# Kernel optimization log

Measured on AMD Instinct MI355X. Metric: run time of the kernel, lower is better.

The kernel has to match this reference:

```python
import jax, jax.numpy as jnp
import numpy as np

B, IN, H, OUT, RANK = 2048, 256, 128, 128, 8
EPS = 1e-5

def setup_inputs() -> dict:
    key = jax.random.key(0)
    ks = jax.random.split(key, 9)
    inv = lambda n: 1.0 / np.sqrt(n)
    return {
        "X": jax.random.normal(ks[0], (B, IN), jnp.float32),
        "W1": jax.random.uniform(ks[1], (IN, H), jnp.float32, -inv(IN), inv(IN)),
        "b1": jnp.zeros((H,), jnp.float32),
        "W2": jax.random.uniform(ks[2], (IN, OUT), jnp.float32, -inv(IN), inv(IN)),
        "b2": jnp.zeros((OUT,), jnp.float32),
        "W3": jax.random.uniform(ks[3], (H, OUT), jnp.float32, -inv(H), inv(H)),
        "b3": jnp.zeros((OUT,), jnp.float32),
        "P": jax.random.normal(ks[4], (RANK, H, H, H), jnp.float32),  # (rank, p, q, k)
        "gz": jnp.ones((H,), jnp.float32),
        "bz": jnp.zeros((H,), jnp.float32),
        "gy": jnp.ones((H,), jnp.float32),
        "by": jnp.zeros((H,), jnp.float32),
    }

def _bn(x, g, b):
    # training-mode BatchNorm1d: batch stats, biased variance
    m = x.mean(axis=0)
    v = x.var(axis=0)
    return (x - m) * jax.lax.rsqrt(v + EPS) * g + b

def reference(X, W1, b1, W2, b2, W3, b3, P, gz, bz, gy, by):
    Z = jax.nn.relu(X @ W1 + b1)               # (B, H); dropout = identity (eval)

    def step(carry, Pi):
        Zi, Y = carry
        # batch_quadratic: out[b,k] = sum_{p,q} Zi[b,p] * Pi[p,q,k] * Z[b,q]
        Zi = jnp.einsum('bp,pqk,bq->bk', Zi, Pi, Z)
        Zi = _bn(Zi, gz, bz)
        return (Zi, Y + Zi / RANK), None

    Y0 = jnp.zeros((X.shape[0], H), X.dtype)
    (_, Y), _ = jax.lax.scan(step, (Z, Y0), P)
    Y = _bn(Y, gy, by)
    out = jax.nn.relu(jax.nn.relu(Y @ W3 + b3) + jax.nn.relu(X @ W2 + b2))
    return out
```

## Files before the change

### kernel.cpp

```cpp
#include <hip/hip_runtime.h>

typedef __bf16 bf16x8 __attribute__((ext_vector_type(8)));
typedef float  floatx4 __attribute__((ext_vector_type(4)));

constexpr int B_    = 2048;
constexpr int NIN   = 256;
constexpr int H_    = 128;
constexpr int RANK_ = 8;
constexpr float EPS_ = 1e-5f;
constexpr int MT    = 32;
constexpr int SZS   = 36;

__global__ __launch_bounds__(256)
void k_head(const float* __restrict__ X,
            const float* __restrict__ W1, const float* __restrict__ b1,
            const float* __restrict__ W2, const float* __restrict__ b2,
            const float* __restrict__ P,
            float* __restrict__ Z, float* __restrict__ R2, __bf16* __restrict__ Zbf,
            __bf16* __restrict__ Pperm, float* __restrict__ stats ) {
    __shared__ float smem[512];
    const int bx = blockIdx.x, t = threadIdx.x;

    if (bx < RANK_ + 1) stats[bx * 256 + t] = 0.f;

    if (bx < 512) {
        const int col = t & 127, half = t >> 7;
        for (int it = 0; it < 2; ++it) {
            const int row0 = bx * 4 + it * 2;
            smem[t]       = X[(size_t)row0       * NIN + t];
            smem[256 + t] = X[(size_t)(row0 + 1) * NIN + t];
            __syncthreads();
            float s1 = 0.f, s2 = 0.f;
            const float* sx = smem + half * 256;
#pragma unroll 8
            for (int i = 0; i < NIN; ++i) {
                s1 = fmaf(sx[i], W1[i * H_ + col], s1);
                s2 = fmaf(sx[i], W2[i * H_ + col], s2);
            }
            const int b = row0 + half;
            const float z = fmaxf(s1 + b1[col], 0.f);
            const float r = fmaxf(s2 + b2[col], 0.f);
            Z[(size_t)b * H_ + col]   = z;
            Zbf[(size_t)b * H_ + col] = (__bf16)z;
            R2[(size_t)b * H_ + col]  = r;
            __syncthreads();
        }
    }
    {
        const int s = t >> 6, Lp = t & 63, quad = Lp >> 4, lo = Lp & 15;
        const int pr = bx >> 7, p = bx & 127;
        const float* Pp = P     + ((size_t)pr * H_ + p) * (H_ * H_);
        __bf16*      dp = Pperm + ((size_t)pr * H_ + p) * (H_ * H_);
#pragma unroll
        for (int c = 0; c < 8; ++c) {
            __bf16 v[8];
#pragma unroll
            for (int jj = 0; jj < 8; ++jj)
                v[jj] = (__bf16)Pp[(s * 32 + quad * 8 + jj) * H_ + c * 16 + lo];
            *(bf16x8*)(dp + (((size_t)(s * 8 + c)) * 64 + Lp) * 8) = *(const bf16x8*)v;
        }
    }
}

__global__ __launch_bounds__(256, 2)
void k_rank(const __bf16* __restrict__ Pr, const __bf16* __restrict__ Zbf,
            const float* __restrict__ prevT, const float* __restrict__ prevStats,
            const float* __restrict__ gz, const float* __restrict__ bz,
            float* __restrict__ T, float* __restrict__ stats, const int first) {
    __shared__ float smem[4864];
    const int m = blockIdx.x, kg = blockIdx.y, b0 = m * MT;
    const int t = threadIdx.x;
    const int w = t >> 6, L = t & 63, quad = L >> 4, lo = L & 15;
    const int sp = t & 127, rg = t >> 7;

    float* sAl = smem + 4608; float* sBe = smem + 4736;
    if (t < 128) {
        if (first) { sAl[t] = 1.f; sBe[t] = 0.f; }
        else {
            const float s1 = prevStats[t], s2 = prevStats[128 + t];
            const float mm = s1 * (1.f / B_);
            const float var = s2 * (1.f / B_) - mm * mm;
            const float a = rsqrtf(var + EPS_) * gz[t];
            sAl[t] = a; sBe[t] = bz[t] - mm * a;
        }
    }
    bf16x8 A[2][4];
#pragma unroll
    for (int mt = 0; mt < 2; ++mt)
#pragma unroll
        for (int ks = 0; ks < 4; ++ks)
            A[mt][ks] = *(const bf16x8*)(Zbf + (size_t)(b0 + mt * 16 + lo) * H_ + ks * 32 + quad * 8);
    __syncthreads();
    {
        const float a = sAl[sp], be = sBe[sp];
#pragma unroll
        for (int i = 0; i < 16; ++i) {
            const int row = rg + 2 * i;
            smem[sp * SZS + row] = fmaf(prevT[(size_t)(b0 + row) * H_ + sp], a, be);
        }
    }
    __syncthreads();

    floatx4 acc[2];
    acc[0] = (floatx4){0.f, 0.f, 0.f, 0.f};
    acc[1] = (floatx4){0.f, 0.f, 0.f, 0.f};
    const bf16x8* Pb = (const bf16x8*)Pr;
    for (int pp = 0; pp < 32; ++pp) {
        const int p = pp * 4 + w;
        bf16x8 Bf[4];
#pragma unroll
        for (int s = 0; s < 4; ++s)
            Bf[s] = Pb[((size_t)(p * 4 + s) * 8 + kg) * 64 + L];
        floatx4 S[2];
        S[0] = (floatx4){0.f, 0.f, 0.f, 0.f};
        S[1] = (floatx4){0.f, 0.f, 0.f, 0.f};
#pragma unroll
        for (int ks = 0; ks < 4; ++ks)
#pragma unroll
            for (int mt = 0; mt < 2; ++mt)
                S[mt] = __builtin_amdgcn_mfma_f32_16x16x32_bf16(A[mt][ks], Bf[ks], S[mt], 0, 0, 0);
#pragma unroll
        for (int mt = 0; mt < 2; ++mt) {
            const floatx4 zi = *(const floatx4*)&smem[p * SZS + mt * 16 + quad * 4];
            acc[mt] += zi * S[mt];
        }
    }
    __syncthreads();
#pragma unroll
    for (int mt = 0; mt < 2; ++mt)
#pragma unroll
        for (int i = 0; i < 4; ++i)
            smem[w * 512 + (mt * 4 + i) * 64 + L] = acc[mt][i];
    if (t < 32) smem[2048 + t] = 0.f;
    __syncthreads();

    float cs = 0.f, cs2 = 0.f;
#pragma unroll
    for (int k2 = 0; k2 < 2; ++k2) {
        const int e = t + 256 * k2;
        const float v = smem[e] + smem[512 + e] + smem[1024 + e] + smem[1536 + e];
        const int j = e >> 6, L2 = e & 63;
        const int row = b0 + (j >> 2) * 16 + (L2 >> 4) * 4 + (j & 3);
        const int col = kg * 16 + (L2 & 15);
        T[(size_t)row * H_ + col] = v;
        cs += v; cs2 += v * v;
    }
    cs  += __shfl_xor(cs, 16);  cs  += __shfl_xor(cs, 32);
    cs2 += __shfl_xor(cs2, 16); cs2 += __shfl_xor(cs2, 32);
    if (L < 16) { atomicAdd(&smem[2048 + L], cs); atomicAdd(&smem[2064 + L], cs2); }
    __syncthreads();
    if (t < 16)      atomicAdd(&stats[kg * 16 + t],            smem[2048 + t]);
    else if (t < 32) atomicAdd(&stats[128 + kg * 16 + t - 16], smem[2048 + t]);
}

__global__ __launch_bounds__(256)
void k_y(const float* __restrict__ T, const float* __restrict__ sums,
         const float* __restrict__ gz, const float* __restrict__ bz,
         float* __restrict__ Y, float* __restrict__ ysums) {
    __shared__ float al[1024], be[1024], red[256];
    const int bx = blockIdx.x, t = threadIdx.x;
    for (int e = t; e < 1024; e += 256) {
        const int rr = e >> 7, k = e & 127;
        const float s1 = sums[rr * 256 + k], s2 = sums[rr * 256 + 128 + k];
        const float mm = s1 * (1.f / B_);
        const float var = s2 * (1.f / B_) - mm * mm;
        const float a = rsqrtf(var + EPS_) * gz[k];
        al[e] = a; be[e] = bz[k] - mm * a;
    }
    red[t] = 0.f;
    __syncthreads();
    const int col = t & 127, half = t >> 7;
    float ps = 0.f, ps2 = 0.f;
    for (int i = 0; i < 16; ++i) {
        const int b = bx * 32 + half + 2 * i;
        float y = 0.f;
#pragma unroll
        for (int rr = 0; rr < 8; ++rr)
            y += fmaf(T[(size_t)rr * B_ * H_ + (size_t)b * H_ + col],
                      al[rr * 128 + col], be[rr * 128 + col]);
        y *= (1.f / RANK_);
        Y[(size_t)b * H_ + col] = y;
        ps += y; ps2 += y * y;
    }
    atomicAdd(&red[col], half == 0 ? ps : 0.f);
    atomicAdd(&red[128 + col], half == 0 ? ps2 : 0.f);
    __syncthreads();
    atomicAdd(&red[col],       half == 1 ? ps : 0.f);
    atomicAdd(&red[128 + col], half == 1 ? ps2 : 0.f);
    __syncthreads();
    if (t < 128) {
        atomicAdd(&ysums[t],       red[t]);
        atomicAdd(&ysums[128 + t], red[128 + t]);
    }
}

__global__ void k_out(const float* __restrict__ Y, const float* __restrict__ ystats,
                      const float* __restrict__ gy, const float* __restrict__ by,
                      const float* __restrict__ W3, const float* __restrict__ b3,
                      const float* __restrict__ R2, float* __restrict__ out) {
    __shared__ float sy[H_];
    const int b = blockIdx.x, t = threadIdx.x;
    const float m  = ystats[t] * (1.f / B_);
    const float v  = ystats[128 + t] * (1.f / B_) - m * m;
    const float rs = rsqrtf(v + EPS_);
    sy[t] = (Y[(size_t)b * H_ + t] - m) * rs * gy[t] + by[t];
    __syncthreads();
    float s = 0.f;
#pragma unroll 8
    for (int h = 0; h < H_; ++h)
        s = fmaf(sy[h], W3[h * H_ + t], s);
    const float r = fmaxf(s + b3[t], 0.f) + R2[(size_t)b * H_ + t];
    out[(size_t)b * H_ + t] = fmaxf(r, 0.f);
}

extern "C" void kernel_launch(void* const* d_in, const int* in_sizes, int n_in,
                              void* d_out, int out_size, void* d_ws, size_t ws_size,
                              hipStream_t stream) {
    const float* X  = (const float*)d_in[0];
    const float* W1 = (const float*)d_in[1];
    const float* b1 = (const float*)d_in[2];
    const float* W2 = (const float*)d_in[3];
    const float* b2 = (const float*)d_in[4];
    const float* W3 = (const float*)d_in[5];
    const float* b3 = (const float*)d_in[6];
    const float* P  = (const float*)d_in[7];
    const float* gz = (const float*)d_in[8];
    const float* bz = (const float*)d_in[9];
    const float* gy = (const float*)d_in[10];
    const float* by = (const float*)d_in[11];
    float* out = (float*)d_out;

    const size_t rankElems = (size_t)H_ * H_ * H_;

    char* wsb = (char*)d_ws;
    float* Z      = (float*)wsb;   wsb += (size_t)B_ * H_ * 4;
    float* R2     = (float*)wsb;   wsb += (size_t)B_ * H_ * 4;
    float* Y      = (float*)wsb;   wsb += (size_t)B_ * H_ * 4;
    float* stats  = (float*)wsb;   wsb += (size_t)(RANK_ + 1) * 256 * 4;
    float* T      = (float*)wsb;   wsb += (size_t)RANK_ * B_ * H_ * 4;
    __bf16* Zbf   = (__bf16*)wsb;  wsb += (size_t)B_ * H_ * 2;
    __bf16* Pperm = (__bf16*)wsb;

    float* ysums = stats + RANK_ * 256;

    k_head<<<1024, 256, 0, stream>>>(X, W1, b1, W2, b2, P, Z, R2, Zbf, Pperm, stats);

    for (int r = 0; r < RANK_; ++r) {
        const float* prevT = (r == 0) ? Z : (T + (size_t)(r - 1) * B_ * H_);
        const float* prevS = (r == 0) ? stats : (stats + (r - 1) * 256);
        k_rank<<<dim3(64, 8), 256, 0, stream>>>(Pperm + (size_t)r * rankElems, Zbf,
                                                prevT, prevS, gz, bz,
                                                T + (size_t)r * B_ * H_, stats + r * 256,
                                                r == 0 ? 1 : 0);
    }

    k_y<<<64, 256, 0, stream>>>(T, stats, gz, bz, Y, ysums);
    k_out<<<B_, H_, 0, stream>>>(Y, ysums, gy, by, W3, b3, R2, out);
}
```

Baseline: 334.5 us.

## Retile rank kernel to 1024-thread blocks, coalesce P permute, batch output rows

The rank kernel now uses 1024-thread blocks covering 64 batch rows, with 16 waves split across row tiles and p slices. The grid is reordered so kg varies fastest, and the next P fragments are prefetched into registers to overlap loads with MFMA. The head kernel's P-to-bf16 permutation now reads P with coalesced float4 loads and transposes through shared memory. The head GEMM is spread over all 1024 blocks, and the output kernel handles 8 rows per block to reuse W3 loads. The larger blocks and prefetch registers may lower occupancy, and the launch bound asks for 4 blocks of 1024 threads per CU.

```diff
diff --git a/kernel.cpp b/kernel.cpp
--- a/kernel.cpp
+++ b/kernel.cpp
@@ -8,8 +8,6 @@
 constexpr int H_    = 128;
 constexpr int RANK_ = 8;
 constexpr float EPS_ = 1e-5f;
-constexpr int MT    = 32;
-constexpr int SZS   = 36;
 
 __global__ __launch_bounds__(256)
 void k_head(const float* __restrict__ X,
@@ -18,62 +16,75 @@
             const float* __restrict__ P,
             float* __restrict__ Z, float* __restrict__ R2, __bf16* __restrict__ Zbf,
             __bf16* __restrict__ Pperm, float* __restrict__ stats ) {
-    __shared__ float smem[512];
+    __shared__ __bf16 sT[128 * 40];
+    float* sx = (float*)sT;
     const int bx = blockIdx.x, t = threadIdx.x;
 
     if (bx < RANK_ + 1) stats[bx * 256 + t] = 0.f;
 
-    if (bx < 512) {
+    {
+        const int row0 = bx * 2;
+        sx[t]       = X[(size_t)row0       * NIN + t];
+        sx[256 + t] = X[(size_t)(row0 + 1) * NIN + t];
+        __syncthreads();
         const int col = t & 127, half = t >> 7;
-        for (int it = 0; it < 2; ++it) {
-            const int row0 = bx * 4 + it * 2;
-            smem[t]       = X[(size_t)row0       * NIN + t];
-            smem[256 + t] = X[(size_t)(row0 + 1) * NIN + t];
+        float s1 = 0.f, s2 = 0.f;
+        const float* sxh = sx + half * 256;
+#pragma unroll 8
+        for (int i = 0; i < NIN; ++i) {
+            s1 = fmaf(sxh[i], W1[i * H_ + col], s1);
+            s2 = fmaf(sxh[i], W2[i * H_ + col], s2);
+        }
+        const int b = row0 + half;
+        const float z = fmaxf(s1 + b1[col], 0.f);
+        const float r = fmaxf(s2 + b2[col], 0.f);
+        Z[(size_t)b * H_ + col]   = z;
+        Zbf[(size_t)b * H_ + col] = (__bf16)z;
+        R2[(size_t)b * H_ + col]  = r;
+        __syncthreads();
+    }
+    {
+        const int pr = bx >> 7, p = bx & 127;
+        const float4* Pp4 = (const float4*)(P + ((size_t)pr * H_ + p) * (H_ * H_));
+        __bf16* dp = Pperm + ((size_t)pr * H_ + p) * (H_ * H_);
+        const int L = t & 63, quad = L >> 4, lo = L & 15, c0 = t >> 6;
+#pragma unroll
+        for (int s = 0; s < 4; ++s) {
+#pragma unroll
+            for (int i = 0; i < 4; ++i) {
+                const int idx = i * 256 + t;
+                const int q = idx >> 5, k4 = idx & 31;
+                const float4 v = Pp4[(size_t)(s * 32 + q) * 32 + k4];
+                __bf16* d = sT + (size_t)(k4 * 4) * 40 + q;
+                d[0]   = (__bf16)v.x;
+                d[40]  = (__bf16)v.y;
+                d[80]  = (__bf16)v.z;
+                d[120] = (__bf16)v.w;
+            }
             __syncthreads();
-            float s1 = 0.f, s2 = 0.f;
-            const float* sx = smem + half * 256;
-#pragma unroll 8
-            for (int i = 0; i < NIN; ++i) {
-                s1 = fmaf(sx[i], W1[i * H_ + col], s1);
-                s2 = fmaf(sx[i], W2[i * H_ + col], s2);
+#pragma unroll
+            for (int cc = 0; cc < 2; ++cc) {
+                const int c = c0 + 4 * cc;
+                const bf16x8 v = *(const bf16x8*)&sT[(c * 16 + lo) * 40 + quad * 8];
+                *(bf16x8*)(dp + (((size_t)(s * 8 + c)) * 64 + L) * 8) = v;
             }
-            const int b = row0 + half;
-            const float z = fmaxf(s1 + b1[col], 0.f);
-            const float r = fmaxf(s2 + b2[col], 0.f);
-            Z[(size_t)b * H_ + col]   = z;
-            Zbf[(size_t)b * H_ + col] = (__bf16)z;
-            R2[(size_t)b * H_ + col]  = r;
             __syncthreads();
         }
     }
-    {
-        const int s = t >> 6, Lp = t & 63, quad = Lp >> 4, lo = Lp & 15;
-        const int pr = bx >> 7, p = bx & 127;
-        const float* Pp = P     + ((size_t)pr * H_ + p) * (H_ * H_);
-        __bf16*      dp = Pperm + ((size_t)pr * H_ + p) * (H_ * H_);
-#pragma unroll
-        for (int c = 0; c < 8; ++c) {
-            __bf16 v[8];
-#pragma unroll
-            for (int jj = 0; jj < 8; ++jj)
-                v[jj] = (__bf16)Pp[(s * 32 + quad * 8 + jj) * H_ + c * 16 + lo];
-            *(bf16x8*)(dp + (((size_t)(s * 8 + c)) * 64 + Lp) * 8) = *(const bf16x8*)v;
-        }
-    }
-}
-
-__global__ __launch_bounds__(256, 2)
+}
+
+__global__ __launch_bounds__(1024, 4)
 void k_rank(const __bf16* __restrict__ Pr, const __bf16* __restrict__ Zbf,
             const float* __restrict__ prevT, const float* __restrict__ prevStats,
             const float* __restrict__ gz, const float* __restrict__ bz,
             float* __restrict__ T, float* __restrict__ stats, const int first) {
-    __shared__ float smem[4864];
-    const int m = blockIdx.x, kg = blockIdx.y, b0 = m * MT;
+    __shared__ float smem[8960];
+    const int kg = blockIdx.x, mblk = blockIdx.y, b0 = mblk * 64;
     const int t = threadIdx.x;
     const int w = t >> 6, L = t & 63, quad = L >> 4, lo = L & 15;
-    const int sp = t & 127, rg = t >> 7;
-
-    float* sAl = smem + 4608; float* sBe = smem + 4736;
+    const int wr = w >> 2, wp = w & 3;
+
+    float* sAl = smem + 8704; float* sBe = smem + 8832;
     if (t < 128) {
         if (first) { sAl[t] = 1.f; sBe[t] = 0.f; }
         else {
@@ -84,73 +95,69 @@
             sAl[t] = a; sBe[t] = bz[t] - mm * a;
         }
     }
-    bf16x8 A[2][4];
-#pragma unroll
-    for (int mt = 0; mt < 2; ++mt)
+    bf16x8 A[4];
+#pragma unroll
+    for (int ks = 0; ks < 4; ++ks)
+        A[ks] = *(const bf16x8*)(Zbf + (size_t)(b0 + wr * 16 + lo) * H_ + ks * 32 + quad * 8);
+    __syncthreads();
+    {
+        const int sp = t & 127, rr = t >> 7;
+        const float a = sAl[sp], be = sBe[sp];
+#pragma unroll
+        for (int i = 0; i < 8; ++i) {
+            const int row = rr + 8 * i;
+            smem[sp * 68 + row] = fmaf(prevT[(size_t)(b0 + row) * H_ + sp], a, be);
+        }
+    }
+    __syncthreads();
+
+    floatx4 acc = (floatx4){0.f, 0.f, 0.f, 0.f};
+    const bf16x8* Pb = (const bf16x8*)Pr;
+    bf16x8 Bf[4], Bn[4];
+#pragma unroll
+    for (int s = 0; s < 4; ++s)
+        Bf[s] = Pb[((size_t)((wp * 4 + s) * 8 + kg)) * 64 + L];
+#pragma unroll 2
+    for (int pp = 0; pp < 32; ++pp) {
+        const int p = pp * 4 + wp;
+        if (pp < 31) {
+            const int pn = p + 4;
+#pragma unroll
+            for (int s = 0; s < 4; ++s)
+                Bn[s] = Pb[((size_t)((pn * 4 + s) * 8 + kg)) * 64 + L];
+        }
+        floatx4 S = (floatx4){0.f, 0.f, 0.f, 0.f};
 #pragma unroll
         for (int ks = 0; ks < 4; ++ks)
-            A[mt][ks] = *(const bf16x8*)(Zbf + (size_t)(b0 + mt * 16 + lo) * H_ + ks * 32 + quad * 8);
-    __syncthreads();
-    {
-        const float a = sAl[sp], be = sBe[sp];
-#pragma unroll
-        for (int i = 0; i < 16; ++i) {
-            const int row = rg + 2 * i;
-            smem[sp * SZS + row] = fmaf(prevT[(size_t)(b0 + row) * H_ + sp], a, be);
-        }
-    }
-    __syncthreads();
-
-    floatx4 acc[2];
-    acc[0] = (floatx4){0.f, 0.f, 0.f, 0.f};
-    acc[1] = (floatx4){0.f, 0.f, 0.f, 0.f};
-    const bf16x8* Pb = (const bf16x8*)Pr;
-    for (int pp = 0; pp < 32; ++pp) {
-        const int p = pp * 4 + w;
-        bf16x8 Bf[4];
-#pragma unroll
-        for (int s = 0; s < 4; ++s)
-            Bf[s] = Pb[((size_t)(p * 4 + s) * 8 + kg) * 64 + L];
-        floatx4 S[2];
-        S[0] = (floatx4){0.f, 0.f, 0.f, 0.f};
-        S[1] = (floatx4){0.f, 0.f, 0.f, 0.f};
-#pragma unroll
-        for (int ks = 0; ks < 4; ++ks)
-#pragma unroll
-            for (int mt = 0; mt < 2; ++mt)
-                S[mt] = __builtin_amdgcn_mfma_f32_16x16x32_bf16(A[mt][ks], Bf[ks], S[mt], 0, 0, 0);
-#pragma unroll
-        for (int mt = 0; mt < 2; ++mt) {
-            const floatx4 zi = *(const floatx4*)&smem[p * SZS + mt * 16 + quad * 4];
-            acc[mt] += zi * S[mt];
-        }
-    }
-    __syncthreads();
-#pragma unroll
-    for (int mt = 0; mt < 2; ++mt)
-#pragma unroll
-        for (int i = 0; i < 4; ++i)
-            smem[w * 512 + (mt * 4 + i) * 64 + L] = acc[mt][i];
-    if (t < 32) smem[2048 + t] = 0.f;
-    __syncthreads();
-
-    float cs = 0.f, cs2 = 0.f;
-#pragma unroll
-    for (int k2 = 0; k2 < 2; ++k2) {
-        const int e = t + 256 * k2;
-        const float v = smem[e] + smem[512 + e] + smem[1024 + e] + smem[1536 + e];
-        const int j = e >> 6, L2 = e & 63;
-        const int row = b0 + (j >> 2) * 16 + (L2 >> 4) * 4 + (j & 3);
-        const int col = kg * 16 + (L2 & 15);
-        T[(size_t)row * H_ + col] = v;
-        cs += v; cs2 += v * v;
-    }
+            S = __builtin_amdgcn_mfma_f32_16x16x32_bf16(A[ks], Bf[ks], S, 0, 0, 0);
+        const floatx4 zi = *(const floatx4*)&smem[p * 68 + wr * 16 + quad * 4];
+        acc += zi * S;
+#pragma unroll
+        for (int s = 0; s < 4; ++s) Bf[s] = Bn[s];
+    }
+    __syncthreads();
+#pragma unroll
+    for (int i = 0; i < 4; ++i)
+        smem[((wr * 4 + wp) * 4 + i) * 64 + L] = acc[i];
+    if (t < 32) smem[4096 + t] = 0.f;
+    __syncthreads();
+
+    const int g = t >> 6, L2 = t & 63;
+    const int wr2 = g >> 2, i2 = g & 3;
+    const int row = b0 + wr2 * 16 + (L2 >> 4) * 4 + i2;
+    const int col = kg * 16 + (L2 & 15);
+    float v = 0.f;
+#pragma unroll
+    for (int q = 0; q < 4; ++q)
+        v += smem[((wr2 * 4 + q) * 4 + i2) * 64 + L2];
+    T[(size_t)row * H_ + col] = v;
+    float cs = v, cs2 = v * v;
     cs  += __shfl_xor(cs, 16);  cs  += __shfl_xor(cs, 32);
     cs2 += __shfl_xor(cs2, 16); cs2 += __shfl_xor(cs2, 32);
-    if (L < 16) { atomicAdd(&smem[2048 + L], cs); atomicAdd(&smem[2064 + L], cs2); }
-    __syncthreads();
-    if (t < 16)      atomicAdd(&stats[kg * 16 + t],            smem[2048 + t]);
-    else if (t < 32) atomicAdd(&stats[128 + kg * 16 + t - 16], smem[2048 + t]);
+    if (L2 < 16) { atomicAdd(&smem[4096 + L2], cs); atomicAdd(&smem[4112 + L2], cs2); }
+    __syncthreads();
+    if (t < 16)      atomicAdd(&stats[kg * 16 + t],            smem[4096 + t]);
+    else if (t < 32) atomicAdd(&stats[128 + kg * 16 + t - 16], smem[4096 + t]);
 }
 
 __global__ __launch_bounds__(256)
@@ -182,10 +189,10 @@
         Y[(size_t)b * H_ + col] = y;
         ps += y; ps2 += y * y;
     }
-    atomicAdd(&red[col], half == 0 ? ps : 0.f);
+    atomicAdd(&red[col],       half == 0 ? ps  : 0.f);
     atomicAdd(&red[128 + col], half == 0 ? ps2 : 0.f);
     __syncthreads();
-    atomicAdd(&red[col],       half == 1 ? ps : 0.f);
+    atomicAdd(&red[col],       half == 1 ? ps  : 0.f);
     atomicAdd(&red[128 + col], half == 1 ? ps2 : 0.f);
     __syncthreads();
     if (t < 128) {
@@ -194,23 +201,36 @@
     }
 }
 
-__global__ void k_out(const float* __restrict__ Y, const float* __restrict__ ystats,
-                      const float* __restrict__ gy, const float* __restrict__ by,
-                      const float* __restrict__ W3, const float* __restrict__ b3,
-                      const float* __restrict__ R2, float* __restrict__ out) {
-    __shared__ float sy[H_];
-    const int b = blockIdx.x, t = threadIdx.x;
-    const float m  = ystats[t] * (1.f / B_);
-    const float v  = ystats[128 + t] * (1.f / B_) - m * m;
-    const float rs = rsqrtf(v + EPS_);
-    sy[t] = (Y[(size_t)b * H_ + t] - m) * rs * gy[t] + by[t];
-    __syncthreads();
-    float s = 0.f;
+__global__ __launch_bounds__(256)
+void k_out(const float* __restrict__ Y, const float* __restrict__ ystats,
+           const float* __restrict__ gy, const float* __restrict__ by,
+           const float* __restrict__ W3, const float* __restrict__ b3,
+           const float* __restrict__ R2, float* __restrict__ out) {
+    __shared__ float sy[8 * 132];
+    const int bx = blockIdx.x, t = threadIdx.x;
+    const int col = t & 127, rh = t >> 7;
+    const int b0 = bx * 8;
+    const float mm = ystats[col] * (1.f / B_);
+    const float var = ystats[128 + col] * (1.f / B_) - mm * mm;
+    const float ay = rsqrtf(var + EPS_) * gy[col];
+    const float bb = by[col] - mm * ay;
+#pragma unroll
+    for (int i = 0; i < 4; ++i) {
+        const int row = rh + 2 * i;
+        sy[row * 132 + col] = fmaf(Y[(size_t)(b0 + row) * H_ + col], ay, bb);
+    }
+    __syncthreads();
+#pragma unroll
+    for (int j = 0; j < 4; ++j) {
+        const int row = rh * 4 + j;
+        float s = 0.f;
+        const float* syr = sy + row * 132;
 #pragma unroll 8
-    for (int h = 0; h < H_; ++h)
-        s = fmaf(sy[h], W3[h * H_ + t], s);
-    const float r = fmaxf(s + b3[t], 0.f) + R2[(size_t)b * H_ + t];
-    out[(size_t)b * H_ + t] = fmaxf(r, 0.f);
+        for (int h = 0; h < H_; ++h)
+            s = fmaf(syr[h], W3[h * H_ + col], s);
+        const size_t gi = (size_t)(b0 + row) * H_ + col;
+        out[gi] = fmaxf(fmaxf(s + b3[col], 0.f) + R2[gi], 0.f);
+    }
 }
 
 extern "C" void kernel_launch(void* const* d_in, const int* in_sizes, int n_in,
@@ -248,12 +268,12 @@
     for (int r = 0; r < RANK_; ++r) {
         const float* prevT = (r == 0) ? Z : (T + (size_t)(r - 1) * B_ * H_);
         const float* prevS = (r == 0) ? stats : (stats + (r - 1) * 256);
-        k_rank<<<dim3(64, 8), 256, 0, stream>>>(Pperm + (size_t)r * rankElems, Zbf,
-                                                prevT, prevS, gz, bz,
-                                                T + (size_t)r * B_ * H_, stats + r * 256,
-                                                r == 0 ? 1 : 0);
+        k_rank<<<dim3(8, 32), 1024, 0, stream>>>(Pperm + (size_t)r * rankElems, Zbf,
+                                                 prevT, prevS, gz, bz,
+                                                 T + (size_t)r * B_ * H_, stats + r * 256,
+                                                 r == 0 ? 1 : 0);
     }
 
     k_y<<<64, 256, 0, stream>>>(T, stats, gz, bz, Y, ysums);
-    k_out<<<B_, H_, 0, stream>>>(Y, ysums, gy, by, W3, b3, R2, out);
-}
+    k_out<<<256, 256, 0, stream>>>(Y, ysums, gy, by, W3, b3, R2, out);
+}
```

Measured after the change: 357.5 us. 1.07x slower.
